# Performance work log

Measured on AMD Instinct MI355X. Metric: run time of the kernel, lower is better.

Reference implementation:

```python
import jax, jax.numpy as jnp
import numpy as np

B, T, C, H = 4, 1024, 1024, 16
HD = C // H
EPS = 1e-5


def _layernorm(x, w, b):
    mu = jnp.mean(x, axis=-1, keepdims=True)
    var = jnp.mean(jnp.square(x - mu), axis=-1, keepdims=True)
    return (x - mu) * jax.lax.rsqrt(var + EPS) * w + b


def setup_inputs() -> dict:
    key = jax.random.key(0)
    ks = jax.random.split(key, 10)
    s = 0.02
    return {
        "x": jax.random.normal(ks[0], (B, T, C), jnp.float32),
        "attention_mask": jnp.zeros((1, 1, T, T), jnp.float32),
        "ln1_w": jnp.ones((C,), jnp.float32),
        "ln1_b": jnp.zeros((C,), jnp.float32),
        "w_qkv": s * jax.random.normal(ks[1], (3 * C, C), jnp.float32),
        "b_qkv": jnp.zeros((3 * C,), jnp.float32),
        "w_o": s * jax.random.normal(ks[2], (C, C), jnp.float32),
        "b_o": jnp.zeros((C,), jnp.float32),
        "ln2_w": jnp.ones((C,), jnp.float32),
        "ln2_b": jnp.zeros((C,), jnp.float32),
        "w_fc": s * jax.random.normal(ks[3], (4 * C, C), jnp.float32),
        "b_fc": jnp.zeros((4 * C,), jnp.float32),
        "w_proj": s * jax.random.normal(ks[4], (C, 4 * C), jnp.float32),
        "b_proj": jnp.zeros((C,), jnp.float32),
    }


def reference(x, attention_mask, ln1_w, ln1_b, w_qkv, b_qkv, w_o, b_o,
              ln2_w, ln2_b, w_fc, b_fc, w_proj, b_proj):
    # --- self-attention on ln_1(x) ---
    h = _layernorm(x, ln1_w, ln1_b)
    qkv = h @ w_qkv.T + b_qkv                      # [B,T,3C]
    q, k, v = jnp.split(qkv, 3, axis=-1)
    q = q.reshape(B, T, H, HD).transpose(0, 2, 1, 3)  # [B,H,T,HD]
    k = k.reshape(B, T, H, HD).transpose(0, 2, 1, 3)
    v = v.reshape(B, T, H, HD).transpose(0, 2, 1, 3)
    att = jnp.einsum('bhqd,bhkd->bhqk', q, k) * (1.0 / np.sqrt(HD))
    att = att + attention_mask
    att_weights = jax.nn.softmax(att, axis=-1)     # [B,H,T,T]
    y = jnp.einsum('bhqk,bhkd->bhqd', att_weights, v)
    y = y.transpose(0, 2, 1, 3).reshape(B, T, C)
    y = y @ w_o.T + b_o
    x = x + y
    # --- MLP on ln_2(x), residual ---
    residual = x
    h2 = _layernorm(x, ln2_w, ln2_b)
    h2 = jax.nn.gelu(h2 @ w_fc.T + b_fc, approximate=False)
    h2 = h2 @ w_proj.T + b_proj
    x = residual + h2
    return (x, att_weights)
```

## Files before the change

### kernel.cpp

```cpp
#include <hip/hip_runtime.h>
#include <stdint.h>
#include <math.h>

typedef __attribute__((ext_vector_type(4))) float f32x4;
typedef __attribute__((ext_vector_type(8))) short s16x8;
typedef __attribute__((ext_vector_type(4))) unsigned short u16x4;

__device__ __forceinline__ unsigned short f2b(float x) {
    union { float f; uint32_t u; } v; v.f = x;
    uint32_t r = v.u + 0x7FFFu + ((v.u >> 16) & 1u);
    return (unsigned short)(r >> 16);
}
__device__ __forceinline__ float b2f(unsigned short u) {
    union { uint32_t u; float f; } v; v.u = (uint32_t)u << 16;
    return v.f;
}

__device__ __forceinline__ void gload16(const unsigned short* g, unsigned short* l) {
    __builtin_amdgcn_global_load_lds(
        (const __attribute__((address_space(1))) unsigned int*)(const void*)g,
        (__attribute__((address_space(3))) unsigned int*)(void*)l,
        16, 0, 0);
}

__device__ __forceinline__ float gelu_t(float u) {
    float z = 0.7978845608f * (u + 0.044715f * u * u * u);
    float ez = __expf(2.0f * z);
    float th = 1.0f - 2.0f / (ez + 1.0f);
    return 0.5f * u * (1.0f + th);
}

__global__ __launch_bounds__(256) void castln_kernel(
        const float* __restrict__ x, const float* __restrict__ lw,
        const float* __restrict__ lb, unsigned short* __restrict__ lout,
        const float* __restrict__ a, int na, const float* __restrict__ b, int nb,
        const float* __restrict__ c, int nc, const float* __restrict__ d, int nd,
        unsigned short* __restrict__ oa, unsigned short* __restrict__ ob,
        unsigned short* __restrict__ oc, unsigned short* __restrict__ od) {
    const int tid = threadIdx.x;
    if (blockIdx.x < 4096) {
        const long row = blockIdx.x;
        f32x4 v = *(const f32x4*)(x + row * 1024 + tid * 4);
        float s  = v[0] + v[1] + v[2] + v[3];
        float sq = v[0]*v[0] + v[1]*v[1] + v[2]*v[2] + v[3]*v[3];
        #pragma unroll
        for (int off = 32; off; off >>= 1) {
            s  += __shfl_xor(s, off);
            sq += __shfl_xor(sq, off);
        }
        __shared__ float red[8];
        if ((tid & 63) == 0) { red[tid >> 6] = s; red[4 + (tid >> 6)] = sq; }
        __syncthreads();
        s  = red[0] + red[1] + red[2] + red[3];
        sq = red[4] + red[5] + red[6] + red[7];
        float mu  = s * (1.0f / 1024.0f);
        float var = sq * (1.0f / 1024.0f) - mu * mu;
        float rs  = rsqrtf(var + 1e-5f);
        f32x4 wv = *(const f32x4*)(lw + tid * 4);
        f32x4 bv = *(const f32x4*)(lb + tid * 4);
        u16x4 o;
        #pragma unroll
        for (int j = 0; j < 4; ++j) o[j] = f2b((v[j] - mu) * rs * wv[j] + bv[j]);
        *(u16x4*)(lout + row * 1024 + tid * 4) = o;
    } else {
        int i = (blockIdx.x - 4096) * 256 + tid;
        const float* src; unsigned short* dst; int off;
        if (i < na)                { src = a; dst = oa; off = i; }
        else if (i < na+nb)        { src = b; dst = ob; off = i - na; }
        else if (i < na+nb+nc)     { src = c; dst = oc; off = i - na - nb; }
        else if (i < na+nb+nc+nd)  { src = d; dst = od; off = i - na - nb - nc; }
        else return;
        f32x4 v = ((const f32x4*)src)[off];
        u16x4 o;
        #pragma unroll
        for (int j = 0; j < 4; ++j) o[j] = f2b(v[j]);
        ((u16x4*)dst)[off] = o;
    }
}

__global__ __launch_bounds__(256) void ln_kernel(const float* __restrict__ x,
                                                 const float* __restrict__ w,
                                                 const float* __restrict__ b,
                                                 unsigned short* __restrict__ out) {
    const long row = blockIdx.x;
    const int tid = threadIdx.x;
    f32x4 v = *(const f32x4*)(x + row * 1024 + tid * 4);
    float s  = v[0] + v[1] + v[2] + v[3];
    float sq = v[0]*v[0] + v[1]*v[1] + v[2]*v[2] + v[3]*v[3];
    #pragma unroll
    for (int off = 32; off; off >>= 1) {
        s  += __shfl_xor(s, off);
        sq += __shfl_xor(sq, off);
    }
    __shared__ float red[8];
    if ((tid & 63) == 0) { red[tid >> 6] = s; red[4 + (tid >> 6)] = sq; }
    __syncthreads();
    s  = red[0] + red[1] + red[2] + red[3];
    sq = red[4] + red[5] + red[6] + red[7];
    float mu  = s * (1.0f / 1024.0f);
    float var = sq * (1.0f / 1024.0f) - mu * mu;
    float rs  = rsqrtf(var + 1e-5f);
    f32x4 wv = *(const f32x4*)(w + tid * 4);
    f32x4 bv = *(const f32x4*)(b + tid * 4);
    u16x4 o;
    #pragma unroll
    for (int j = 0; j < 4; ++j) o[j] = f2b((v[j] - mu) * rs * wv[j] + bv[j]);
    *(u16x4*)(out + row * 1024 + tid * 4) = o;
}

__global__ __launch_bounds__(256)
void pv_att(const unsigned short* __restrict__ E,
            const unsigned short* __restrict__ Vt,
            const float* __restrict__ psum,
            float* __restrict__ att,
            unsigned short* __restrict__ y) {
    __shared__ unsigned short ldsA[3][64 * 32];
    __shared__ unsigned short ldsB[3][64 * 32];
    __shared__ float invl_s[64];
    const int tid = threadIdx.x, lane = tid & 63, wid = tid >> 6;
    const int wr = wid >> 1, wc = wid & 1;
    const int bh = blockIdx.y;
    const int q0 = blockIdx.x * 64;
    const int fr = lane & 15, fs = lane >> 4;

    const unsigned short* Ab = E + ((long)bh << 20) + (long)q0 * 1024;
    const unsigned short* Bb = Vt + ((long)bh << 16);

    const int e0  = wid * 512 + lane * 8;
    const int r0a = e0 >> 5, c0a = e0 & 31;
    float* attRow = att + ((long)bh << 20) + (long)(q0 + r0a) * 1024 + c0a;

    f32x4 acc[2][2] = {};

#define PSTAGE(T, BUF)                                                        \
    {                                                                         \
        const int k0s = (T) << 5;                                             \
        gload16(Ab + k0s + (long)r0a * 1024 + c0a, &ldsA[BUF][wid * 512]);    \
        gload16(Bb + k0s + (long)r0a * 1024 + c0a, &ldsB[BUF][wid * 512]);    \
    }

    PSTAGE(0, 0);
    PSTAGE(1, 1);

    if (tid < 64) {
        const float* p = psum + ((((long)bh << 10) + q0 + tid) << 4);
        f32x4 pa = *(const f32x4*)p,       pb = *(const f32x4*)(p + 4);
        f32x4 pc = *(const f32x4*)(p + 8), pd = *(const f32x4*)(p + 12);
        float s = (pa[0]+pa[1]+pa[2]+pa[3]) + (pb[0]+pb[1]+pb[2]+pb[3])
                + (pc[0]+pc[1]+pc[2]+pc[3]) + (pd[0]+pd[1]+pd[2]+pd[3]);
        invl_s[tid] = 1.0f / s;
    }

    for (int t = 0; t < 32; ++t) {
        const int buf = t % 3;
        if (t == 0)       asm volatile("s_waitcnt vmcnt(2)" ::: "memory");
        else if (t == 1)  asm volatile("s_waitcnt vmcnt(4)" ::: "memory");
        else if (t < 31)  asm volatile("s_waitcnt vmcnt(6)" ::: "memory");
        else              asm volatile("s_waitcnt vmcnt(4)" ::: "memory");
        __syncthreads();
        if (t + 2 < 32) PSTAGE(t + 2, (t + 2) % 3);

        {
            const float il_a = invl_s[r0a];
            s16x8 ea = *(const s16x8*)&ldsA[buf][e0];
            f32x4 o0, o1;
            #pragma unroll
            for (int j = 0; j < 4; ++j) o0[j] = b2f((unsigned short)ea[j]) * il_a;
            #pragma unroll
            for (int j = 0; j < 4; ++j) o1[j] = b2f((unsigned short)ea[4 + j]) * il_a;
            *(f32x4*)(attRow + t * 32)     = o0;
            *(f32x4*)(attRow + t * 32 + 4) = o1;
        }

        s16x8 af[2], vb[2];
        #pragma unroll
        for (int m = 0; m < 2; ++m)
            af[m] = *(const s16x8*)&ldsA[buf][(wr * 32 + m * 16 + fr) * 32 + fs * 8];
        #pragma unroll
        for (int n = 0; n < 2; ++n)
            vb[n] = *(const s16x8*)&ldsB[buf][(wc * 32 + n * 16 + fr) * 32 + fs * 8];
        #pragma unroll
        for (int m = 0; m < 2; ++m)
            #pragma unroll
            for (int n = 0; n < 2; ++n)
                acc[m][n] = __builtin_amdgcn_mfma_f32_16x16x32_bf16(af[m], vb[n], acc[m][n], 0, 0, 0);
    }
#undef PSTAGE

    const int bb = bh >> 4, hh = bh & 15;
    #pragma unroll
    for (int m = 0; m < 2; ++m) {
        #pragma unroll
        for (int r = 0; r < 4; ++r) {
            const int lrow = wr * 32 + m * 16 + fs * 4 + r;
            const float il = invl_s[lrow];
            const int trow = q0 + lrow;
            #pragma unroll
            for (int n = 0; n < 2; ++n) {
                const int c = hh * 64 + wc * 32 + n * 16 + fr;
                y[((long)(bb * 1024 + trow) << 10) + c] = f2b(acc[m][n][r] * il);
            }
        }
    }
}

template <int BM, int BN, int EPI>
__global__ __launch_bounds__(256)
void gemm_bt(const unsigned short* __restrict__ A,
             const unsigned short* __restrict__ Bm,
             int K, int lda, int ldb, int ldc,
             long sAz, long sBz,
             const float* __restrict__ bias,
             const float* __restrict__ resid,
             float* __restrict__ outF,
             unsigned short* __restrict__ outB) {
    constexpr int WM = BM / 2, WN = BN / 2;
    constexpr int FM = WM / 16, FN = WN / 16;
    constexpr int NTA = BM / 64, NTB = BN / 64;
    constexpr int LOADS = NTA + NTB;
    constexpr int STR = 136;
    constexpr int STRF = 132;
    __shared__ unsigned short shm[3 * BM * 32 + 3 * BN * 32];
    unsigned short* ldsA = shm;
    unsigned short* ldsB = shm + 3 * BM * 32;

    const int tid  = threadIdx.x;
    const int lane = tid & 63;
    const int wid  = tid >> 6;
    const int wr   = wid >> 1, wc = wid & 1;
    const int bz   = blockIdx.z;
    const int row0 = blockIdx.x * BM;
    const int col0 = blockIdx.y * BN;

    const unsigned short* Ab = A + (long)bz * sAz + (long)row0 * lda;
    const unsigned short* Bb = Bm + (long)bz * sBz + (long)col0 * ldb;

    const int nt = K >> 5;
    f32x4 acc[FM][FN] = {};
    const int fr = lane & 15;
    const int fk = (lane >> 4) * 8;

#define STAGE(T, BUF)                                                              \
    {                                                                              \
        const int k0s = (T) << 5;                                                  \
        _Pragma("unroll")                                                          \
        for (int i = 0; i < NTA; ++i) {                                            \
            int e = i * 2048 + wid * 512 + lane * 8;                               \
            gload16(Ab + k0s + (long)(e >> 5) * lda + (e & 31),                    \
                    &ldsA[(BUF) * BM * 32 + i * 2048 + wid * 512]);                \
        }                                                                          \
        _Pragma("unroll")                                                          \
        for (int i = 0; i < NTB; ++i) {                                            \
            int e = i * 2048 + wid * 512 + lane * 8;                               \
            gload16(Bb + k0s + (long)(e >> 5) * ldb + (e & 31),                    \
                    &ldsB[(BUF) * BN * 32 + i * 2048 + wid * 512]);                \
        }                                                                          \
    }

    STAGE(0, 0);
    if (nt > 1) STAGE(1, 1);

    for (int t = 0; t < nt; ++t) {
        const int buf = t % 3;
        if (t + 1 < nt) {
            if constexpr (LOADS == 2)      asm volatile("s_waitcnt vmcnt(2)" ::: "memory");
            else if constexpr (LOADS == 3) asm volatile("s_waitcnt vmcnt(3)" ::: "memory");
            else                           asm volatile("s_waitcnt vmcnt(4)" ::: "memory");
        } else {
            asm volatile("s_waitcnt vmcnt(0)" ::: "memory");
        }
        __syncthreads();
        if (t + 2 < nt) STAGE(t + 2, (t + 2) % 3);

        s16x8 af[FM], bfr[FN];
        #pragma unroll
        for (int m = 0; m < FM; ++m)
            af[m] = *(const s16x8*)&ldsA[buf * BM * 32 + (wr * WM + m * 16 + fr) * 32 + fk];
        #pragma unroll
        for (int n = 0; n < FN; ++n)
            bfr[n] = *(const s16x8*)&ldsB[buf * BN * 32 + (wc * WN + n * 16 + fr) * 32 + fk];
        #pragma unroll
        for (int m = 0; m < FM; ++m)
            #pragma unroll
            for (int n = 0; n < FN; ++n)
                acc[m][n] = __builtin_amdgcn_mfma_f32_16x16x32_bf16(af[m], bfr[n], acc[m][n], 0, 0, 0);
    }
#undef STAGE

    const int cj = lane & 15;
    const int r0 = (lane >> 4) * 4;

    if constexpr (EPI == 1) {
        __syncthreads();
        #pragma unroll
        for (int m = 0; m < FM; ++m) {
            #pragma unroll
            for (int r = 0; r < 4; ++r) {
                const int prow = wr * WM + m * 16 + r0 + r;
                const int grow = row0 + prow;
                float rs = 0.0f;
                #pragma unroll
                for (int n = 0; n < FN; ++n) {
                    const int pcol = wc * WN + n * 16 + cj;
                    float e = __expf(acc[m][n][r] + resid[((long)grow << 10) + col0 + pcol]);
                    rs += e;
                    shm[prow * STR + pcol] = f2b(e);
                }
                rs += __shfl_xor(rs, 1); rs += __shfl_xor(rs, 2);
                rs += __shfl_xor(rs, 4); rs += __shfl_xor(rs, 8);
                if (cj == 0)
                    outF[((((long)bz << 10) + grow) << 4) + blockIdx.y * 2 + wc] = rs;
            }
        }
        __syncthreads();
        #pragma unroll
        for (int j = 0; j < 8; ++j) {
            const int idx = j * 2048 + tid * 8;
            const int row = idx >> 7, c = idx & 127;
            s16x8 val = *(const s16x8*)&shm[row * STR + c];
            *(s16x8*)(outB + ((long)bz << 20) + ((long)(row0 + row) << 10) + col0 + c) = val;
        }
    } else if constexpr (EPI == 0) {
        const int seg = col0 >> 10;
        const int bb = row0 >> 10;
        __syncthreads();
        if (seg < 2) {
            #pragma unroll
            for (int m = 0; m < FM; ++m)
                #pragma unroll
                for (int n = 0; n < FN; ++n)
                    #pragma unroll
                    for (int r = 0; r < 4; ++r) {
                        const int prow = wr * WM + m * 16 + r0 + r;
                        const int pcol = wc * WN + n * 16 + cj;
                        float v = acc[m][n][r] + bias[col0 + pcol];
                        if (seg == 0) v *= 0.125f;
                        shm[prow * STR + pcol] = f2b(v);
                    }
            __syncthreads();
            #pragma unroll
            for (int j = 0; j < 8; ++j) {
                const int idx = j * 2048 + tid * 8;
                const int row = idx >> 7, c = idx & 127;
                s16x8 val = *(const s16x8*)&shm[row * STR + c];
                const int t = (row0 + row) & 1023;
                const int hh = ((col0 & 1023) >> 6) + (c >> 6);
                const int dd = c & 63;
                const long bh = bb * 16 + hh;
                *(s16x8*)(outB + (seg == 1 ? 4194304 : 0) + (bh << 16) + (t << 6) + dd) = val;
            }
        } else {
            #pragma unroll
            for (int m = 0; m < FM; ++m)
                #pragma unroll
                for (int n = 0; n < FN; ++n)
                    #pragma unroll
                    for (int r = 0; r < 4; ++r) {
                        const int prow = wr * WM + m * 16 + r0 + r;
                        const int pcol = wc * WN + n * 16 + cj;
                        shm[pcol * 144 + prow] = f2b(acc[m][n][r] + bias[col0 + pcol]);
                    }
            __syncthreads();
            #pragma unroll
            for (int j = 0; j < 8; ++j) {
                const int idx = j * 2048 + tid * 8;
                const int ddl = idx >> 7, tl = idx & 127;
                s16x8 val = *(const s16x8*)&shm[ddl * 144 + tl];
                const int hh = ((col0 & 1023) >> 6) + (ddl >> 6);
                const int dd = ddl & 63;
                const int t = (row0 & 1023) + tl;
                const long bh = bb * 16 + hh;
                *(s16x8*)(outB + 8388608 + (bh << 16) + (dd << 10) + t) = val;
            }
        }
    } else if constexpr (EPI == 4) {
        __syncthreads();
        #pragma unroll
        for (int m = 0; m < FM; ++m)
            #pragma unroll
            for (int n = 0; n < FN; ++n)
                #pragma unroll
                for (int r = 0; r < 4; ++r) {
                    const int prow = wr * WM + m * 16 + r0 + r;
                    const int pcol = wc * WN + n * 16 + cj;
                    float u = acc[m][n][r] + bias[col0 + pcol];
                    shm[prow * STR + pcol] = f2b(gelu_t(u));
                }
        __syncthreads();
        #pragma unroll
        for (int j = 0; j < 8; ++j) {
            const int idx = j * 2048 + tid * 8;
            const int row = idx >> 7, c = idx & 127;
            s16x8 val = *(const s16x8*)&shm[row * STR + c];
            *(s16x8*)(outB + (long)(row0 + row) * ldc + col0 + c) = val;
        }
    } else {
        float* shf = (float*)shm;
        __syncthreads();
        #pragma unroll
        for (int m = 0; m < FM; ++m)
            #pragma unroll
            for (int n = 0; n < FN; ++n)
                #pragma unroll
                for (int r = 0; r < 4; ++r) {
                    const int prow = wr * WM + m * 16 + r0 + r;
                    const int pcol = wc * WN + n * 16 + cj;
                    shf[prow * STRF + pcol] = acc[m][n][r];
                }
        __syncthreads();
        #pragma unroll
        for (int j = 0; j < (BM * BN / 1024); ++j) {
            const int idx = j * 1024 + tid * 4;
            const int row = idx >> 7, c = idx & 127;
            f32x4 v = *(const f32x4*)&shf[row * STRF + c];
            const long gbase = ((long)(row0 + row) << 10) + col0 + c;
            f32x4 bv = *(const f32x4*)(bias + col0 + c);
            f32x4 rv = *(const f32x4*)(resid + gbase);
            #pragma unroll
            for (int q = 0; q < 4; ++q) v[q] += bv[q] + rv[q];
            *(f32x4*)(outF + gbase) = v;
        }
    }
}

extern "C" void kernel_launch(void* const* d_in, const int* in_sizes, int n_in,
                              void* d_out, int out_size, void* d_ws, size_t ws_size,
                              hipStream_t stream) {
    (void)in_sizes; (void)n_in; (void)out_size; (void)ws_size;
    const float* x     = (const float*)d_in[0];
    const float* mask  = (const float*)d_in[1];
    const float* ln1w  = (const float*)d_in[2];
    const float* ln1b  = (const float*)d_in[3];
    const float* wqkv  = (const float*)d_in[4];
    const float* bqkv  = (const float*)d_in[5];
    const float* wo    = (const float*)d_in[6];
    const float* bo    = (const float*)d_in[7];
    const float* ln2w  = (const float*)d_in[8];
    const float* ln2b  = (const float*)d_in[9];
    const float* wfc   = (const float*)d_in[10];
    const float* bfc   = (const float*)d_in[11];
    const float* wproj = (const float*)d_in[12];
    const float* bproj = (const float*)d_in[13];

    float* outx = (float*)d_out;
    float* att  = (float*)d_out + 4194304;

    char* ws = (char*)d_ws;
    unsigned short* h_bf     = (unsigned short*)ws;  ws += (size_t)8  << 20;
    unsigned short* wqkv_bf  = (unsigned short*)ws;  ws += (size_t)6  << 20;
    unsigned short* wo_bf    = (unsigned short*)ws;  ws += (size_t)2  << 20;
    unsigned short* wfc_bf   = (unsigned short*)ws;  ws += (size_t)8  << 20;
    unsigned short* wproj_bf = (unsigned short*)ws;  ws += (size_t)8  << 20;
    unsigned short* q_bf     = (unsigned short*)ws;  ws += (size_t)24 << 20;
    unsigned short* k_bf     = q_bf + 4194304;
    unsigned short* vT_bf    = q_bf + 8388608;
    unsigned short* e_b      = (unsigned short*)ws;  ws += (size_t)128 << 20;
    unsigned short* y_bf     = (unsigned short*)ws;  ws += (size_t)8  << 20;
    float*          x2       = (float*)ws;           ws += (size_t)16 << 20;
    unsigned short* gelu_bf  = (unsigned short*)ws;  ws += (size_t)32 << 20;
    float*          psum     = (float*)ws;           ws += (size_t)4  << 20;

    castln_kernel<<<16384, 256, 0, stream>>>(
        x, ln1w, ln1b, h_bf,
        wqkv, 786432, wo, 262144, wfc, 1048576, wproj, 1048576,
        wqkv_bf, wo_bf, wfc_bf, wproj_bf);

    gemm_bt<128, 128, 0><<<dim3(32, 24, 1), 256, 0, stream>>>(
        h_bf, wqkv_bf, 1024, 1024, 1024, 0, 0, 0,
        bqkv, nullptr, nullptr, q_bf);

    gemm_bt<128, 128, 1><<<dim3(8, 8, 64), 256, 0, stream>>>(
        q_bf, k_bf, 64, 64, 64, 0, 65536, 65536,
        nullptr, mask, psum, e_b);

    pv_att<<<dim3(16, 64), 256, 0, stream>>>(e_b, vT_bf, psum, att, y_bf);

    gemm_bt<64, 128, 3><<<dim3(64, 8, 1), 256, 0, stream>>>(
        y_bf, wo_bf, 1024, 1024, 1024, 1024, 0, 0,
        bo, x, x2, nullptr);

    ln_kernel<<<4096, 256, 0, stream>>>(x2, ln2w, ln2b, h_bf);

    gemm_bt<128, 128, 4><<<dim3(32, 32, 1), 256, 0, stream>>>(
        h_bf, wfc_bf, 1024, 1024, 1024, 4096, 0, 0,
        bfc, nullptr, nullptr, gelu_bf);

    gemm_bt<64, 128, 3><<<dim3(64, 8, 1), 256, 0, stream>>>(
        gelu_bf, wproj_bf, 4096, 4096, 4096, 1024, 0, 0,
        bproj, x2, outx, nullptr);
}
```

Baseline: 414.3 us.

## Recompute QK^T scores in PV kernel instead of storing bf16 exp matrix

The QK^T GEMM now emits only the per-row partial sums of exp(score+mask) and no longer writes the 128 MB bf16 exp buffer. A new attention kernel recomputes Q·K^T per 64-key tile with MFMA, applies the mask and exp, writes the normalized attention weights, and multiplies by V from registers and LDS. This removes a large HBM write and re-read of the intermediate in exchange for computing QK^T and exp twice and reading the mask twice.

```diff
diff --git a/kernel.cpp b/kernel.cpp
--- a/kernel.cpp
+++ b/kernel.cpp
@@ -109,38 +109,20 @@
 }
 
 __global__ __launch_bounds__(256)
-void pv_att(const unsigned short* __restrict__ E,
-            const unsigned short* __restrict__ Vt,
-            const float* __restrict__ psum,
-            float* __restrict__ att,
-            unsigned short* __restrict__ y) {
-    __shared__ unsigned short ldsA[3][64 * 32];
-    __shared__ unsigned short ldsB[3][64 * 32];
+void attn2(const unsigned short* __restrict__ Qg,
+           const unsigned short* __restrict__ Kg,
+           const unsigned short* __restrict__ Vt,
+           const float* __restrict__ mask,
+           const float* __restrict__ psum,
+           float* __restrict__ att,
+           unsigned short* __restrict__ y) {
+    __shared__ unsigned short Ks[2][64][72];
+    __shared__ unsigned short Vs[2][64][72];
+    __shared__ unsigned short Ps[4][16][72];
     __shared__ float invl_s[64];
     const int tid = threadIdx.x, lane = tid & 63, wid = tid >> 6;
-    const int wr = wid >> 1, wc = wid & 1;
-    const int bh = blockIdx.y;
-    const int q0 = blockIdx.x * 64;
     const int fr = lane & 15, fs = lane >> 4;
-
-    const unsigned short* Ab = E + ((long)bh << 20) + (long)q0 * 1024;
-    const unsigned short* Bb = Vt + ((long)bh << 16);
-
-    const int e0  = wid * 512 + lane * 8;
-    const int r0a = e0 >> 5, c0a = e0 & 31;
-    float* attRow = att + ((long)bh << 20) + (long)(q0 + r0a) * 1024 + c0a;
-
-    f32x4 acc[2][2] = {};
-
-#define PSTAGE(T, BUF)                                                        \
-    {                                                                         \
-        const int k0s = (T) << 5;                                             \
-        gload16(Ab + k0s + (long)r0a * 1024 + c0a, &ldsA[BUF][wid * 512]);    \
-        gload16(Bb + k0s + (long)r0a * 1024 + c0a, &ldsB[BUF][wid * 512]);    \
-    }
-
-    PSTAGE(0, 0);
-    PSTAGE(1, 1);
+    const int bh = blockIdx.y, q0 = blockIdx.x * 64;
 
     if (tid < 64) {
         const float* p = psum + ((((long)bh << 10) + q0 + tid) << 4);
@@ -151,56 +133,97 @@
         invl_s[tid] = 1.0f / s;
     }
 
-    for (int t = 0; t < 32; ++t) {
-        const int buf = t % 3;
-        if (t == 0)       asm volatile("s_waitcnt vmcnt(2)" ::: "memory");
-        else if (t == 1)  asm volatile("s_waitcnt vmcnt(4)" ::: "memory");
-        else if (t < 31)  asm volatile("s_waitcnt vmcnt(6)" ::: "memory");
-        else              asm volatile("s_waitcnt vmcnt(4)" ::: "memory");
-        __syncthreads();
-        if (t + 2 < 32) PSTAGE(t + 2, (t + 2) % 3);
-
-        {
-            const float il_a = invl_s[r0a];
-            s16x8 ea = *(const s16x8*)&ldsA[buf][e0];
-            f32x4 o0, o1;
-            #pragma unroll
-            for (int j = 0; j < 4; ++j) o0[j] = b2f((unsigned short)ea[j]) * il_a;
-            #pragma unroll
-            for (int j = 0; j < 4; ++j) o1[j] = b2f((unsigned short)ea[4 + j]) * il_a;
-            *(f32x4*)(attRow + t * 32)     = o0;
-            *(f32x4*)(attRow + t * 32 + 4) = o1;
-        }
-
-        s16x8 af[2], vb[2];
-        #pragma unroll
-        for (int m = 0; m < 2; ++m)
-            af[m] = *(const s16x8*)&ldsA[buf][(wr * 32 + m * 16 + fr) * 32 + fs * 8];
-        #pragma unroll
-        for (int n = 0; n < 2; ++n)
-            vb[n] = *(const s16x8*)&ldsB[buf][(wc * 32 + n * 16 + fr) * 32 + fs * 8];
-        #pragma unroll
-        for (int m = 0; m < 2; ++m)
-            #pragma unroll
-            for (int n = 0; n < 2; ++n)
-                acc[m][n] = __builtin_amdgcn_mfma_f32_16x16x32_bf16(af[m], vb[n], acc[m][n], 0, 0, 0);
-    }
-#undef PSTAGE
+    const unsigned short* qp = Qg + ((long)bh << 16) + (long)(q0 + wid * 16 + fr) * 64 + fs * 8;
+    const s16x8 aq0 = *(const s16x8*)qp;
+    const s16x8 aq1 = *(const s16x8*)(qp + 32);
+
+    const int srow = tid >> 2, scol = (tid & 3) * 16;
+    const unsigned short* kbase = Kg + ((long)bh << 16) + (long)srow * 64 + scol;
+    const unsigned short* vbase = Vt + ((long)bh << 16) + (long)srow * 1024 + scol;
+
+    s16x8 k0a, k0b, v0a, v0b, k1a, k1b, v1a, v1b;
+    k0a = *(const s16x8*)kbase;            k0b = *(const s16x8*)(kbase + 8);
+    v0a = *(const s16x8*)vbase;            v0b = *(const s16x8*)(vbase + 8);
+    k1a = *(const s16x8*)(kbase + 4096);   k1b = *(const s16x8*)(kbase + 4104);
+    v1a = *(const s16x8*)(vbase + 64);     v1b = *(const s16x8*)(vbase + 72);
+
+    f32x4 acc[4] = {};
+
+#define AITER(KT, BUF, KA, KB, VA, VB)                                              \
+    {                                                                               \
+        *(s16x8*)&Ks[BUF][srow][scol]     = KA;                                     \
+        *(s16x8*)&Ks[BUF][srow][scol + 8] = KB;                                     \
+        *(s16x8*)&Vs[BUF][srow][scol]     = VA;                                     \
+        *(s16x8*)&Vs[BUF][srow][scol + 8] = VB;                                     \
+        __syncthreads();                                                            \
+        if ((KT) + 2 < 16) {                                                        \
+            const unsigned short* kp = kbase + (long)((KT) + 2) * 4096;             \
+            const unsigned short* vp = vbase + ((KT) + 2) * 64;                     \
+            KA = *(const s16x8*)kp;  KB = *(const s16x8*)(kp + 8);                  \
+            VA = *(const s16x8*)vp;  VB = *(const s16x8*)(vp + 8);                  \
+        }                                                                           \
+        f32x4 s4[4];                                                                \
+        _Pragma("unroll")                                                           \
+        for (int n = 0; n < 4; ++n) {                                               \
+            s16x8 b0 = *(const s16x8*)&Ks[BUF][n * 16 + fr][fs * 8];                \
+            s16x8 b1 = *(const s16x8*)&Ks[BUF][n * 16 + fr][32 + fs * 8];           \
+            f32x4 z = {};                                                           \
+            z = __builtin_amdgcn_mfma_f32_16x16x32_bf16(aq0, b0, z, 0, 0, 0);       \
+            z = __builtin_amdgcn_mfma_f32_16x16x32_bf16(aq1, b1, z, 0, 0, 0);       \
+            s4[n] = z;                                                              \
+        }                                                                           \
+        _Pragma("unroll")                                                           \
+        for (int r = 0; r < 4; ++r) {                                               \
+            const long mb = ((long)(q0 + wid * 16 + fs * 4 + r) << 10) + (KT) * 64; \
+            _Pragma("unroll")                                                       \
+            for (int n = 0; n < 4; ++n) {                                           \
+                float e = __expf(s4[n][r] + mask[mb + n * 16 + fr]);                \
+                Ps[wid][fs * 4 + r][n * 16 + fr] = f2b(e);                          \
+            }                                                                       \
+        }                                                                           \
+        {                                                                           \
+            const float il = invl_s[srow];                                          \
+            s16x8 p0 = *(const s16x8*)&Ps[wid][srow & 15][scol];                    \
+            s16x8 p1 = *(const s16x8*)&Ps[wid][srow & 15][scol + 8];                \
+            float* ap = att + ((long)bh << 20) + ((long)(q0 + srow) << 10)          \
+                        + (KT) * 64 + scol;                                         \
+            f32x4 o;                                                                \
+            _Pragma("unroll") for (int j = 0; j < 4; ++j) o[j] = b2f((unsigned short)p0[j]) * il; \
+            *(f32x4*)ap = o;                                                        \
+            _Pragma("unroll") for (int j = 0; j < 4; ++j) o[j] = b2f((unsigned short)p0[4 + j]) * il; \
+            *(f32x4*)(ap + 4) = o;                                                  \
+            _Pragma("unroll") for (int j = 0; j < 4; ++j) o[j] = b2f((unsigned short)p1[j]) * il; \
+            *(f32x4*)(ap + 8) = o;                                                  \
+            _Pragma("unroll") for (int j = 0; j < 4; ++j) o[j] = b2f((unsigned short)p1[4 + j]) * il; \
+            *(f32x4*)(ap + 12) = o;                                                 \
+        }                                                                           \
+        {                                                                           \
+            s16x8 pa0 = *(const s16x8*)&Ps[wid][fr][fs * 8];                        \
+            s16x8 pa1 = *(const s16x8*)&Ps[wid][fr][32 + fs * 8];                   \
+            _Pragma("unroll")                                                       \
+            for (int n = 0; n < 4; ++n) {                                           \
+                s16x8 vb0 = *(const s16x8*)&Vs[BUF][n * 16 + fr][fs * 8];           \
+                s16x8 vb1 = *(const s16x8*)&Vs[BUF][n * 16 + fr][32 + fs * 8];      \
+                acc[n] = __builtin_amdgcn_mfma_f32_16x16x32_bf16(pa0, vb0, acc[n], 0, 0, 0); \
+                acc[n] = __builtin_amdgcn_mfma_f32_16x16x32_bf16(pa1, vb1, acc[n], 0, 0, 0); \
+            }                                                                       \
+        }                                                                           \
+    }
+
+    for (int kt2 = 0; kt2 < 16; kt2 += 2) {
+        AITER(kt2,     0, k0a, k0b, v0a, v0b);
+        AITER(kt2 + 1, 1, k1a, k1b, v1a, v1b);
+    }
+#undef AITER
 
     const int bb = bh >> 4, hh = bh & 15;
     #pragma unroll
-    for (int m = 0; m < 2; ++m) {
-        #pragma unroll
-        for (int r = 0; r < 4; ++r) {
-            const int lrow = wr * 32 + m * 16 + fs * 4 + r;
-            const float il = invl_s[lrow];
-            const int trow = q0 + lrow;
-            #pragma unroll
-            for (int n = 0; n < 2; ++n) {
-                const int c = hh * 64 + wc * 32 + n * 16 + fr;
-                y[((long)(bb * 1024 + trow) << 10) + c] = f2b(acc[m][n][r] * il);
-            }
-        }
+    for (int r = 0; r < 4; ++r) {
+        const int q = q0 + wid * 16 + fs * 4 + r;
+        const float il = invl_s[wid * 16 + fs * 4 + r];
+        #pragma unroll
+        for (int n = 0; n < 4; ++n)
+            y[((long)(bb * 1024 + q) << 10) + hh * 64 + n * 16 + fr] = f2b(acc[n][r] * il);
     }
 }
 
@@ -290,35 +313,23 @@
     const int cj = lane & 15;
     const int r0 = (lane >> 4) * 4;
 
-    if constexpr (EPI == 1) {
-        __syncthreads();
+    if constexpr (EPI == 5) {
         #pragma unroll
         for (int m = 0; m < FM; ++m) {
             #pragma unroll
             for (int r = 0; r < 4; ++r) {
-                const int prow = wr * WM + m * 16 + r0 + r;
-                const int grow = row0 + prow;
+                const int grow = row0 + wr * WM + m * 16 + r0 + r;
                 float rs = 0.0f;
                 #pragma unroll
                 for (int n = 0; n < FN; ++n) {
-                    const int pcol = wc * WN + n * 16 + cj;
-                    float e = __expf(acc[m][n][r] + resid[((long)grow << 10) + col0 + pcol]);
-                    rs += e;
-                    shm[prow * STR + pcol] = f2b(e);
+                    const int gcol = col0 + wc * WN + n * 16 + cj;
+                    rs += __expf(acc[m][n][r] + resid[((long)grow << 10) + gcol]);
                 }
                 rs += __shfl_xor(rs, 1); rs += __shfl_xor(rs, 2);
                 rs += __shfl_xor(rs, 4); rs += __shfl_xor(rs, 8);
                 if (cj == 0)
                     outF[((((long)bz << 10) + grow) << 4) + blockIdx.y * 2 + wc] = rs;
             }
-        }
-        __syncthreads();
-        #pragma unroll
-        for (int j = 0; j < 8; ++j) {
-            const int idx = j * 2048 + tid * 8;
-            const int row = idx >> 7, c = idx & 127;
-            s16x8 val = *(const s16x8*)&shm[row * STR + c];
-            *(s16x8*)(outB + ((long)bz << 20) + ((long)(row0 + row) << 10) + col0 + c) = val;
         }
     } else if constexpr (EPI == 0) {
         const int seg = col0 >> 10;
@@ -454,7 +465,6 @@
     unsigned short* q_bf     = (unsigned short*)ws;  ws += (size_t)24 << 20;
     unsigned short* k_bf     = q_bf + 4194304;
     unsigned short* vT_bf    = q_bf + 8388608;
-    unsigned short* e_b      = (unsigned short*)ws;  ws += (size_t)128 << 20;
     unsigned short* y_bf     = (unsigned short*)ws;  ws += (size_t)8  << 20;
     float*          x2       = (float*)ws;           ws += (size_t)16 << 20;
     unsigned short* gelu_bf  = (unsigned short*)ws;  ws += (size_t)32 << 20;
@@ -469,11 +479,12 @@
         h_bf, wqkv_bf, 1024, 1024, 1024, 0, 0, 0,
         bqkv, nullptr, nullptr, q_bf);
 
-    gemm_bt<128, 128, 1><<<dim3(8, 8, 64), 256, 0, stream>>>(
+    gemm_bt<128, 128, 5><<<dim3(8, 8, 64), 256, 0, stream>>>(
         q_bf, k_bf, 64, 64, 64, 0, 65536, 65536,
-        nullptr, mask, psum, e_b);
-
-    pv_att<<<dim3(16, 64), 256, 0, stream>>>(e_b, vT_bf, psum, att, y_bf);
+        nullptr, mask, psum, nullptr);
+
+    attn2<<<dim3(16, 64), 256, 0, stream>>>(
+        q_bf, k_bf, vT_bf, mask, psum, att, y_bf);
 
     gemm_bt<64, 128, 3><<<dim3(64, 8, 1), 256, 0, stream>>>(
         y_bf, wo_bf, 1024, 1024, 1024, 1024, 0, 0,
```

Result: faster. 394.0 us, median of 2 (-4.9%).

## Fuse QK^T, softmax and PV into one two-pass attention kernel

Applied to the files above, without the earlier changes.

Replaces the separate score GEMM (which wrote bf16 exp scores and partial row sums to a 128MB workspace) and the PV kernel with a single kernel. The new kernel computes QK^T twice per query tile: once to get exact row sums, then again to write normalized attention weights and accumulate P·V through a small per-wave LDS tile. This removes the large intermediate round trip through HBM, at the cost of doing the QK^T matmul and exp twice. K and V fragments are read straight from global memory without LDS staging or pipelining.

```diff
diff --git a/kernel.cpp b/kernel.cpp
--- a/kernel.cpp
+++ b/kernel.cpp
@@ -109,98 +109,114 @@
 }
 
 __global__ __launch_bounds__(256)
-void pv_att(const unsigned short* __restrict__ E,
-            const unsigned short* __restrict__ Vt,
-            const float* __restrict__ psum,
-            float* __restrict__ att,
-            unsigned short* __restrict__ y) {
-    __shared__ unsigned short ldsA[3][64 * 32];
-    __shared__ unsigned short ldsB[3][64 * 32];
-    __shared__ float invl_s[64];
+void attn_nb(const unsigned short* __restrict__ Qg,
+             const unsigned short* __restrict__ Kg,
+             const unsigned short* __restrict__ Vt,
+             const float* __restrict__ mask,
+             float* __restrict__ att,
+             unsigned short* __restrict__ y) {
+    __shared__ unsigned short Ps[4][16][72];
+    __shared__ float invl_s[4][16];
     const int tid = threadIdx.x, lane = tid & 63, wid = tid >> 6;
-    const int wr = wid >> 1, wc = wid & 1;
-    const int bh = blockIdx.y;
-    const int q0 = blockIdx.x * 64;
     const int fr = lane & 15, fs = lane >> 4;
-
-    const unsigned short* Ab = E + ((long)bh << 20) + (long)q0 * 1024;
-    const unsigned short* Bb = Vt + ((long)bh << 16);
-
-    const int e0  = wid * 512 + lane * 8;
-    const int r0a = e0 >> 5, c0a = e0 & 31;
-    float* attRow = att + ((long)bh << 20) + (long)(q0 + r0a) * 1024 + c0a;
-
-    f32x4 acc[2][2] = {};
-
-#define PSTAGE(T, BUF)                                                        \
-    {                                                                         \
-        const int k0s = (T) << 5;                                             \
-        gload16(Ab + k0s + (long)r0a * 1024 + c0a, &ldsA[BUF][wid * 512]);    \
-        gload16(Bb + k0s + (long)r0a * 1024 + c0a, &ldsB[BUF][wid * 512]);    \
-    }
-
-    PSTAGE(0, 0);
-    PSTAGE(1, 1);
-
-    if (tid < 64) {
-        const float* p = psum + ((((long)bh << 10) + q0 + tid) << 4);
-        f32x4 pa = *(const f32x4*)p,       pb = *(const f32x4*)(p + 4);
-        f32x4 pc = *(const f32x4*)(p + 8), pd = *(const f32x4*)(p + 12);
-        float s = (pa[0]+pa[1]+pa[2]+pa[3]) + (pb[0]+pb[1]+pb[2]+pb[3])
-                + (pc[0]+pc[1]+pc[2]+pc[3]) + (pd[0]+pd[1]+pd[2]+pd[3]);
-        invl_s[tid] = 1.0f / s;
-    }
-
-    for (int t = 0; t < 32; ++t) {
-        const int buf = t % 3;
-        if (t == 0)       asm volatile("s_waitcnt vmcnt(2)" ::: "memory");
-        else if (t == 1)  asm volatile("s_waitcnt vmcnt(4)" ::: "memory");
-        else if (t < 31)  asm volatile("s_waitcnt vmcnt(6)" ::: "memory");
-        else              asm volatile("s_waitcnt vmcnt(4)" ::: "memory");
-        __syncthreads();
-        if (t + 2 < 32) PSTAGE(t + 2, (t + 2) % 3);
-
+    const int bh = blockIdx.y, q0 = blockIdx.x * 64;
+    const int qw = q0 + wid * 16;
+
+    const unsigned short* qp = Qg + ((long)bh << 16) + (long)(qw + fr) * 64 + fs * 8;
+    const s16x8 aq0 = *(const s16x8*)qp;
+    const s16x8 aq1 = *(const s16x8*)(qp + 32);
+
+    const unsigned short* Kb = Kg + ((long)bh << 16);
+    const unsigned short* Vb = Vt + ((long)bh << 16);
+    const float* mrow = mask + ((long)(qw + fs * 4) << 10);
+
+    float rs4[4] = {0.0f, 0.0f, 0.0f, 0.0f};
+    for (int kt = 0; kt < 16; ++kt) {
+        #pragma unroll
+        for (int n = 0; n < 4; ++n) {
+            const unsigned short* kp = Kb + (long)(kt * 64 + n * 16 + fr) * 64 + fs * 8;
+            s16x8 b0 = *(const s16x8*)kp;
+            s16x8 b1 = *(const s16x8*)(kp + 32);
+            f32x4 z = {};
+            z = __builtin_amdgcn_mfma_f32_16x16x32_bf16(aq0, b0, z, 0, 0, 0);
+            z = __builtin_amdgcn_mfma_f32_16x16x32_bf16(aq1, b1, z, 0, 0, 0);
+            #pragma unroll
+            for (int r = 0; r < 4; ++r)
+                rs4[r] += __expf(z[r] + mrow[((long)r << 10) + kt * 64 + n * 16 + fr]);
+        }
+    }
+    float il4[4];
+    #pragma unroll
+    for (int r = 0; r < 4; ++r) {
+        float t = rs4[r];
+        t += __shfl_xor(t, 1); t += __shfl_xor(t, 2);
+        t += __shfl_xor(t, 4); t += __shfl_xor(t, 8);
+        il4[r] = 1.0f / t;
+    }
+    if (fr == 0) {
+        #pragma unroll
+        for (int r = 0; r < 4; ++r) invl_s[wid][fs * 4 + r] = il4[r];
+    }
+
+    f32x4 acc[4] = {};
+    const int lr = lane >> 2, lc = (lane & 3) * 16;
+    float* attw = att + ((long)bh << 20) + ((long)(qw + lr) << 10) + lc;
+
+    for (int kt = 0; kt < 16; ++kt) {
+        #pragma unroll
+        for (int n = 0; n < 4; ++n) {
+            const unsigned short* kp = Kb + (long)(kt * 64 + n * 16 + fr) * 64 + fs * 8;
+            s16x8 b0 = *(const s16x8*)kp;
+            s16x8 b1 = *(const s16x8*)(kp + 32);
+            f32x4 z = {};
+            z = __builtin_amdgcn_mfma_f32_16x16x32_bf16(aq0, b0, z, 0, 0, 0);
+            z = __builtin_amdgcn_mfma_f32_16x16x32_bf16(aq1, b1, z, 0, 0, 0);
+            #pragma unroll
+            for (int r = 0; r < 4; ++r) {
+                float e = __expf(z[r] + mrow[((long)r << 10) + kt * 64 + n * 16 + fr]);
+                Ps[wid][fs * 4 + r][n * 16 + fr] = f2b(e);
+            }
+        }
         {
-            const float il_a = invl_s[r0a];
-            s16x8 ea = *(const s16x8*)&ldsA[buf][e0];
-            f32x4 o0, o1;
-            #pragma unroll
-            for (int j = 0; j < 4; ++j) o0[j] = b2f((unsigned short)ea[j]) * il_a;
-            #pragma unroll
-            for (int j = 0; j < 4; ++j) o1[j] = b2f((unsigned short)ea[4 + j]) * il_a;
-            *(f32x4*)(attRow + t * 32)     = o0;
-            *(f32x4*)(attRow + t * 32 + 4) = o1;
-        }
-
-        s16x8 af[2], vb[2];
-        #pragma unroll
-        for (int m = 0; m < 2; ++m)
-            af[m] = *(const s16x8*)&ldsA[buf][(wr * 32 + m * 16 + fr) * 32 + fs * 8];
-        #pragma unroll
-        for (int n = 0; n < 2; ++n)
-            vb[n] = *(const s16x8*)&ldsB[buf][(wc * 32 + n * 16 + fr) * 32 + fs * 8];
-        #pragma unroll
-        for (int m = 0; m < 2; ++m)
-            #pragma unroll
-            for (int n = 0; n < 2; ++n)
-                acc[m][n] = __builtin_amdgcn_mfma_f32_16x16x32_bf16(af[m], vb[n], acc[m][n], 0, 0, 0);
-    }
-#undef PSTAGE
+            const float il = invl_s[wid][lr];
+            s16x8 p0 = *(const s16x8*)&Ps[wid][lr][lc];
+            s16x8 p1 = *(const s16x8*)&Ps[wid][lr][lc + 8];
+            float* ap = attw + kt * 64;
+            f32x4 o;
+            #pragma unroll
+            for (int j = 0; j < 4; ++j) o[j] = b2f((unsigned short)p0[j]) * il;
+            *(f32x4*)ap = o;
+            #pragma unroll
+            for (int j = 0; j < 4; ++j) o[j] = b2f((unsigned short)p0[4 + j]) * il;
+            *(f32x4*)(ap + 4) = o;
+            #pragma unroll
+            for (int j = 0; j < 4; ++j) o[j] = b2f((unsigned short)p1[j]) * il;
+            *(f32x4*)(ap + 8) = o;
+            #pragma unroll
+            for (int j = 0; j < 4; ++j) o[j] = b2f((unsigned short)p1[4 + j]) * il;
+            *(f32x4*)(ap + 12) = o;
+        }
+        {
+            s16x8 pa0 = *(const s16x8*)&Ps[wid][fr][fs * 8];
+            s16x8 pa1 = *(const s16x8*)&Ps[wid][fr][32 + fs * 8];
+            #pragma unroll
+            for (int n = 0; n < 4; ++n) {
+                const unsigned short* vp = Vb + (long)(n * 16 + fr) * 1024 + kt * 64 + fs * 8;
+                s16x8 vb0 = *(const s16x8*)vp;
+                s16x8 vb1 = *(const s16x8*)(vp + 32);
+                acc[n] = __builtin_amdgcn_mfma_f32_16x16x32_bf16(pa0, vb0, acc[n], 0, 0, 0);
+                acc[n] = __builtin_amdgcn_mfma_f32_16x16x32_bf16(pa1, vb1, acc[n], 0, 0, 0);
+            }
+        }
+    }
 
     const int bb = bh >> 4, hh = bh & 15;
     #pragma unroll
-    for (int m = 0; m < 2; ++m) {
-        #pragma unroll
-        for (int r = 0; r < 4; ++r) {
-            const int lrow = wr * 32 + m * 16 + fs * 4 + r;
-            const float il = invl_s[lrow];
-            const int trow = q0 + lrow;
-            #pragma unroll
-            for (int n = 0; n < 2; ++n) {
-                const int c = hh * 64 + wc * 32 + n * 16 + fr;
-                y[((long)(bb * 1024 + trow) << 10) + c] = f2b(acc[m][n][r] * il);
-            }
-        }
+    for (int r = 0; r < 4; ++r) {
+        const int q = qw + fs * 4 + r;
+        #pragma unroll
+        for (int n = 0; n < 4; ++n)
+            y[((long)(bb * 1024 + q) << 10) + hh * 64 + n * 16 + fr] = f2b(acc[n][r] * il4[r]);
     }
 }
 
@@ -290,37 +306,7 @@
     const int cj = lane & 15;
     const int r0 = (lane >> 4) * 4;
 
-    if constexpr (EPI == 1) {
-        __syncthreads();
-        #pragma unroll
-        for (int m = 0; m < FM; ++m) {
-            #pragma unroll
-            for (int r = 0; r < 4; ++r) {
-                const int prow = wr * WM + m * 16 + r0 + r;
-                const int grow = row0 + prow;
-                float rs = 0.0f;
-                #pragma unroll
-                for (int n = 0; n < FN; ++n) {
-                    const int pcol = wc * WN + n * 16 + cj;
-                    float e = __expf(acc[m][n][r] + resid[((long)grow << 10) + col0 + pcol]);
-                    rs += e;
-                    shm[prow * STR + pcol] = f2b(e);
-                }
-                rs += __shfl_xor(rs, 1); rs += __shfl_xor(rs, 2);
-                rs += __shfl_xor(rs, 4); rs += __shfl_xor(rs, 8);
-                if (cj == 0)
-                    outF[((((long)bz << 10) + grow) << 4) + blockIdx.y * 2 + wc] = rs;
-            }
-        }
-        __syncthreads();
-        #pragma unroll
-        for (int j = 0; j < 8; ++j) {
-            const int idx = j * 2048 + tid * 8;
-            const int row = idx >> 7, c = idx & 127;
-            s16x8 val = *(const s16x8*)&shm[row * STR + c];
-            *(s16x8*)(outB + ((long)bz << 20) + ((long)(row0 + row) << 10) + col0 + c) = val;
-        }
-    } else if constexpr (EPI == 0) {
+    if constexpr (EPI == 0) {
         const int seg = col0 >> 10;
         const int bb = row0 >> 10;
         __syncthreads();
@@ -454,11 +440,9 @@
     unsigned short* q_bf     = (unsigned short*)ws;  ws += (size_t)24 << 20;
     unsigned short* k_bf     = q_bf + 4194304;
     unsigned short* vT_bf    = q_bf + 8388608;
-    unsigned short* e_b      = (unsigned short*)ws;  ws += (size_t)128 << 20;
     unsigned short* y_bf     = (unsigned short*)ws;  ws += (size_t)8  << 20;
     float*          x2       = (float*)ws;           ws += (size_t)16 << 20;
     unsigned short* gelu_bf  = (unsigned short*)ws;  ws += (size_t)32 << 20;
-    float*          psum     = (float*)ws;           ws += (size_t)4  << 20;
 
     castln_kernel<<<16384, 256, 0, stream>>>(
         x, ln1w, ln1b, h_bf,
@@ -469,11 +453,8 @@
         h_bf, wqkv_bf, 1024, 1024, 1024, 0, 0, 0,
         bqkv, nullptr, nullptr, q_bf);
 
-    gemm_bt<128, 128, 1><<<dim3(8, 8, 64), 256, 0, stream>>>(
-        q_bf, k_bf, 64, 64, 64, 0, 65536, 65536,
-        nullptr, mask, psum, e_b);
-
-    pv_att<<<dim3(16, 64), 256, 0, stream>>>(e_b, vT_bf, psum, att, y_bf);
+    attn_nb<<<dim3(16, 64), 256, 0, stream>>>(
+        q_bf, k_bf, vT_bf, mask, att, y_bf);
 
     gemm_bt<64, 128, 3><<<dim3(64, 8, 1), 256, 0, stream>>>(
         y_bf, wo_bf, 1024, 1024, 1024, 1024, 0, 0,
```

Result: slower. 473.5 us (+14.3%).
